# Performance work log

Measured on AMD Instinct MI355X. Metric: run time of the kernel, lower is better.

The kernel has to match this reference:

```python
import jax, jax.numpy as jnp
import numpy as np

HQ, HKV, HD = 32, 8, 64
ROPE_BASE = 10000.0


def _rope_cos_sin(L):
    # torchtune-style interleaved RoPE cache
    theta = 1.0 / (ROPE_BASE ** (jnp.arange(0, HD, 2, dtype=jnp.float32) / HD))  # [HD/2]
    ang = jnp.arange(L, dtype=jnp.float32)[:, None] * theta[None, :]             # [L, HD/2]
    return jnp.cos(ang)[None, :, None, :], jnp.sin(ang)[None, :, None, :]        # [1,L,1,HD/2]


def _apply_rope(t, cos, sin):
    # t: [B, L, H, HD]; pairs are interleaved along last dim
    x = t.reshape(t.shape[:-1] + (HD // 2, 2))
    x0, x1 = x[..., 0], x[..., 1]
    out = jnp.stack([x0 * cos - x1 * sin, x1 * cos + x0 * sin], axis=-1)
    return out.reshape(t.shape)


def setup_inputs() -> dict:
    key = jax.random.key(0)
    k1, k2, k3 = jax.random.split(key, 3)
    B, L, D = 2, 2048, 2048
    x = jax.random.normal(k1, (B, L, D), dtype=jnp.float32)
    w_qkv = jax.random.normal(k2, ((HQ + 2 * HKV) * HD, D), dtype=jnp.float32) * 0.02
    w_o = jax.random.normal(k3, (D, D), dtype=jnp.float32) * 0.02
    return {"x": x, "w_qkv": w_qkv, "w_o": w_o}


def reference(x, w_qkv, w_o):
    B, L, D = x.shape
    G = HQ // HKV  # q heads per kv head
    qkv = x @ w_qkv.T  # [B, L, (HQ+2*HKV)*HD]
    q = qkv[..., : HQ * HD].reshape(B, L, HQ, HD)
    k = qkv[..., HQ * HD : (HQ + HKV) * HD].reshape(B, L, HKV, HD)
    v = qkv[..., (HQ + HKV) * HD :].reshape(B, L, HKV, HD)

    cos, sin = _rope_cos_sin(L)
    q = _apply_rope(q, cos, sin)
    k = _apply_rope(k, cos, sin)

    # GQA: q head h attends with kv head h // G
    q = q.transpose(0, 2, 1, 3).reshape(B, HKV, G, L, HD)
    k = k.transpose(0, 2, 1, 3)  # [B, HKV, L, HD]
    v = v.transpose(0, 2, 1, 3)

    scale = 1.0 / jnp.sqrt(jnp.float32(HD))
    scores = jnp.einsum('bhgqd,bhkd->bhgqk', q, k) * scale  # [B,HKV,G,L,L]
    causal = jnp.tril(jnp.ones((L, L), dtype=bool))
    scores = jnp.where(causal, scores, jnp.finfo(scores.dtype).min)
    attn = jax.nn.softmax(scores, axis=-1)
    y = jnp.einsum('bhgqk,bhkd->bhgqd', attn, v)            # [B,HKV,G,L,HD]
    y = y.reshape(B, HQ, L, HD).transpose(0, 2, 1, 3).reshape(B, L, D)
    return y @ w_o.T
```

## Files before the change

kernel.cpp:

```cpp
#include <hip/hip_runtime.h>

typedef __attribute__((ext_vector_type(8))) short bf16x8;
typedef __attribute__((ext_vector_type(4))) float f32x4;

__device__ __forceinline__ float bf2f(unsigned short u) {
  unsigned int x = ((unsigned int)u) << 16;
  float f; __builtin_memcpy(&f, &x, 4); return f;
}
__device__ __forceinline__ unsigned short f2bf(float f) {
  unsigned int x; __builtin_memcpy(&x, &f, 4);
  unsigned int lsb = (x >> 16) & 1u;
  x += 0x7fffu + lsb;
  return (unsigned short)(x >> 16);
}
__device__ __forceinline__ unsigned short f2bf_trunc(float f) {
  unsigned int x; __builtin_memcpy(&x, &f, 4);
  return (unsigned short)(x >> 16);
}
__device__ __forceinline__ float exp2_raw(float x) {
  float r;
  asm("v_exp_f32 %0, %1" : "=v"(r) : "v"(x));
  return r;
}
__device__ __forceinline__ void gload16(const unsigned short* g, unsigned short* l) {
  __builtin_amdgcn_global_load_lds(
      (const __attribute__((address_space(1))) unsigned int*)g,
      (__attribute__((address_space(3))) unsigned int*)l, 16, 0, 0);
}

__global__ __launch_bounds__(256) void cvt3(const float* __restrict__ x,
                                            const float* __restrict__ wq,
                                            const float* __restrict__ wo,
                                            unsigned short* __restrict__ xb,
                                            unsigned short* __restrict__ wqb,
                                            unsigned short* __restrict__ wob) {
  const int N0 = 1048576, N1 = 786432, N2 = 524288;
  for (int i = blockIdx.x * 256 + threadIdx.x; i < N0 + N1 + N2;
       i += (int)(gridDim.x * 256)) {
    const float* in; unsigned short* out; int j;
    if (i < N0)            { in = x;  out = xb;  j = i; }
    else if (i < N0 + N1)  { in = wq; out = wqb; j = i - N0; }
    else                   { in = wo; out = wob; j = i - N0 - N1; }
    const float4* p = (const float4*)(in + (size_t)j * 8);
    float4 a = p[0], b = p[1];
    union { bf16x8 v; unsigned short u[8]; } o;
    o.u[0] = f2bf(a.x); o.u[1] = f2bf(a.y); o.u[2] = f2bf(a.z); o.u[3] = f2bf(a.w);
    o.u[4] = f2bf(b.x); o.u[5] = f2bf(b.y); o.u[6] = f2bf(b.z); o.u[7] = f2bf(b.w);
    *(bf16x8*)(out + (size_t)j * 8) = o.v;
  }
}

template <int F32OUT>
__global__ __launch_bounds__(256) void gemm_bt(const unsigned short* __restrict__ A,
                                               const unsigned short* __restrict__ B,
                                               void* __restrict__ Cp, int N) {
  __shared__ unsigned short sA[128 * 64];
  __shared__ unsigned short sB[128 * 64];
  const int t = threadIdx.x;
  const int lane = t & 63, w = t >> 6;
  const int wm = w >> 1, wn = w & 1;
  const int l16 = lane & 15, hi = lane >> 4;
  const int m0 = blockIdx.y * 128, n0 = blockIdx.x * 128;

  f32x4 zero = {0.f, 0.f, 0.f, 0.f};
  f32x4 acc[4][4];
#pragma unroll
  for (int mi = 0; mi < 4; ++mi)
#pragma unroll
    for (int ni = 0; ni < 4; ++ni) acc[mi][ni] = zero;

  const unsigned short* gA = A + (size_t)m0 * 2048;
  const unsigned short* gB = B + (size_t)n0 * 2048;

  for (int k0 = 0; k0 < 2048; k0 += 64) {
    __syncthreads();
#pragma unroll
    for (int i = 0; i < 4; ++i) {
      int c = i * 256 + t;
      int row = c >> 3, cb = c & 7;
      gload16(gA + (size_t)row * 2048 + k0 + ((cb ^ (row & 7)) * 8), &sA[c * 8]);
    }
#pragma unroll
    for (int i = 0; i < 4; ++i) {
      int c = i * 256 + t;
      int row = c >> 3, cb = c & 7;
      gload16(gB + (size_t)row * 2048 + k0 + ((cb ^ (row & 7)) * 8), &sB[c * 8]);
    }
    __syncthreads();
#pragma unroll
    for (int kk = 0; kk < 2; ++kk) {
      bf16x8 af[4], bfr[4];
#pragma unroll
      for (int i = 0; i < 4; ++i) {
        int rowa = wm * 64 + i * 16 + l16;
        af[i]  = *(const bf16x8*)&sA[rowa * 64 + (((kk * 4 + hi) ^ (l16 & 7)) * 8)];
        int rowb = wn * 64 + i * 16 + l16;
        bfr[i] = *(const bf16x8*)&sB[rowb * 64 + (((kk * 4 + hi) ^ (l16 & 7)) * 8)];
      }
#pragma unroll
      for (int mi = 0; mi < 4; ++mi)
#pragma unroll
        for (int ni = 0; ni < 4; ++ni)
          acc[mi][ni] = __builtin_amdgcn_mfma_f32_16x16x32_bf16(af[mi], bfr[ni], acc[mi][ni], 0, 0, 0);
    }
  }

  const int rowb = m0 + wm * 64 + hi * 4;
  const int colb = n0 + wn * 64 + l16;
#pragma unroll
  for (int mi = 0; mi < 4; ++mi)
#pragma unroll
    for (int ni = 0; ni < 4; ++ni)
#pragma unroll
      for (int r = 0; r < 4; ++r) {
        size_t idx = (size_t)(rowb + mi * 16 + r) * N + colb + ni * 16;
        if (F32OUT) ((float*)Cp)[idx] = acc[mi][ni][r];
        else        ((unsigned short*)Cp)[idx] = f2bf(acc[mi][ni][r]);
      }
}

__global__ __launch_bounds__(256) void prep(const unsigned short* __restrict__ qkv,
                                            unsigned short* __restrict__ q,
                                            unsigned short* __restrict__ k,
                                            unsigned short* __restrict__ vt) {
  __shared__ unsigned short sT[64 * 72];
  const int bid = blockIdx.x;
  if (bid < 640) {
    int tid = bid * 256 + threadIdx.x;
    int l = tid & 2047;
    int rest = tid >> 11;
    int b = rest & 1;
    int h = rest >> 1;
    const unsigned short* src = qkv + (size_t)(b * 2048 + l) * 3072 + h * 64;
    union { uint4 v[8]; unsigned short u[64]; } buf;
#pragma unroll
    for (int i = 0; i < 8; ++i) buf.v[i] = ((const uint4*)src)[i];
    const float sc = (h < 32) ? 0.125f * 1.44269504088896f : 1.0f;
#pragma unroll
    for (int j = 0; j < 32; ++j) {
      float fr = exp2f(-(float)j * 0.41524101186092033f);
      float ang = (float)l * fr;
      float sn, cs;
      sincosf(ang, &sn, &cs);
      float x0 = bf2f(buf.u[2 * j]), x1 = bf2f(buf.u[2 * j + 1]);
      float y0 = (x0 * cs - x1 * sn) * sc;
      float y1 = (x1 * cs + x0 * sn) * sc;
      buf.u[2 * j] = f2bf(y0);
      buf.u[2 * j + 1] = f2bf(y1);
    }
    unsigned short* dst = (h < 32) ? (q + ((size_t)(b * 32 + h) * 2048 + l) * 64)
                                   : (k + ((size_t)(b * 8 + h - 32) * 2048 + l) * 64);
#pragma unroll
    for (int i = 0; i < 8; ++i) ((uint4*)dst)[i] = buf.v[i];
  } else {
    const int bid2 = bid - 640;
    const int xb = bid2 & 31, bh = bid2 >> 5;
    const int t = threadIdx.x;
    const int b = bh >> 3, h = bh & 7;
    const int l0 = xb * 64;
    const int c = t & 7, i0 = t >> 3;
#pragma unroll
    for (int pp = 0; pp < 2; ++pp) {
      int i = i0 + pp * 32;
      const unsigned short* src =
          qkv + (size_t)(b * 2048 + l0 + i) * 3072 + 2560 + h * 64 + c * 8;
      union { bf16x8 v; unsigned short u[8]; } x;
      x.v = *(const bf16x8*)src;
#pragma unroll
      for (int e = 0; e < 8; ++e) sT[(c * 8 + e) * 72 + i] = x.u[e];
    }
    __syncthreads();
    const int d = t >> 2, ic = (t & 3) * 16;
    unsigned short* dst = vt + ((size_t)(b * 8 + h) * 64 + d) * 2048 + l0 + ic;
    *(bf16x8*)dst = *(const bf16x8*)&sT[d * 72 + ic];
    *(bf16x8*)(dst + 8) = *(const bf16x8*)&sT[d * 72 + ic + 8];
  }
}

__global__ __launch_bounds__(256) void attn(const unsigned short* __restrict__ Q,
                                            const unsigned short* __restrict__ K,
                                            const unsigned short* __restrict__ VT,
                                            unsigned short* __restrict__ Y) {
  __shared__ unsigned short sK[128 * 64];
  __shared__ unsigned short sV[64 * 128];
  __shared__ unsigned short sP[4][32 * 136];
  const int t = threadIdx.x, lane = t & 63, w = t >> 6;
  const int l16 = lane & 15, hi = lane >> 4;
  const int pi = blockIdx.y;
  const int bx = blockIdx.x;
  const int head = ((bx & 7) << 3) | (bx >> 3);
  const int b = head >> 5, hq = head & 31, hkv = hq >> 2;
  const unsigned short* kp = K + (size_t)(b * 8 + hkv) * 2048 * 64;
  const unsigned short* vp = VT + (size_t)(b * 8 + hkv) * 64 * 2048;
  unsigned short* sPw = sP[w];
  f32x4 zero = {0.f, 0.f, 0.f, 0.f};
  union { bf16x8 v; unsigned short u[8]; } ones_u;
#pragma unroll
  for (int j = 0; j < 8; ++j) ones_u.u[j] = 0x3F80;
  const bf16x8 ones = ones_u.v;

#pragma unroll
  for (int phase = 0; phase < 2; ++phase) {
    const int qb = phase ? (15 - pi) : pi;
    const int q0 = qb * 128 + w * 32;
    const unsigned short* qp = Q + ((size_t)(b * 32 + hq) * 2048 + q0) * 64;

    bf16x8 qf[2][2];
#pragma unroll
    for (int mi = 0; mi < 2; ++mi)
#pragma unroll
      for (int ks = 0; ks < 2; ++ks)
        qf[mi][ks] = *(const bf16x8*)(qp + (size_t)(mi * 16 + l16) * 64 + ks * 32 + hi * 8);

    f32x4 o[2][4];
    f32x4 os[2];
#pragma unroll
    for (int mi = 0; mi < 2; ++mi) {
#pragma unroll
      for (int ni = 0; ni < 4; ++ni) o[mi][ni] = zero;
      os[mi] = zero;
    }

    const int nt = qb + 1;
    for (int tt = 0; tt < nt; ++tt) {
      const int c0 = tt * 128;
      __syncthreads();
#pragma unroll
      for (int i = 0; i < 4; ++i) {
        int c = i * 256 + t;
        int row = c >> 3, cb = c & 7;
        gload16(kp + (size_t)(c0 + row) * 64 + ((cb ^ (row & 7)) * 8), &sK[c * 8]);
      }
#pragma unroll
      for (int i = 0; i < 4; ++i) {
        int c = i * 256 + t;
        int d = c >> 4, cb = c & 15;
        gload16(vp + (size_t)d * 2048 + c0 + ((cb ^ (d & 15)) * 8), &sV[c * 8]);
      }
      __syncthreads();

#pragma unroll
      for (int h = 0; h < 2; ++h) {
        const int c0h = c0 + h * 64;
        if (c0h > q0) break;
        f32x4 sc[2][4];
#pragma unroll
        for (int mi = 0; mi < 2; ++mi)
#pragma unroll
          for (int ni = 0; ni < 4; ++ni) sc[mi][ni] = zero;
#pragma unroll
        for (int ni = 0; ni < 4; ++ni) {
          const int krow = h * 64 + ni * 16 + l16;
          bf16x8 k0f = *(const bf16x8*)&sK[krow * 64 + ((hi ^ (l16 & 7)) * 8)];
          bf16x8 k1f = *(const bf16x8*)&sK[krow * 64 + (((4 + hi) ^ (l16 & 7)) * 8)];
#pragma unroll
          for (int mi = 0; mi < 2; ++mi) {
            sc[mi][ni] = __builtin_amdgcn_mfma_f32_16x16x32_bf16(qf[mi][0], k0f, sc[mi][ni], 0, 0, 0);
            sc[mi][ni] = __builtin_amdgcn_mfma_f32_16x16x32_bf16(qf[mi][1], k1f, sc[mi][ni], 0, 0, 0);
          }
        }
        if (c0h + 64 > q0) {
#pragma unroll
          for (int mi = 0; mi < 2; ++mi)
#pragma unroll
            for (int ni = 0; ni < 4; ++ni)
#pragma unroll
              for (int r = 0; r < 4; ++r) {
                int col = c0h + ni * 16 + l16;
                int row = q0 + mi * 16 + hi * 4 + r;
                if (col > row) sc[mi][ni][r] = -1e30f;
              }
        }
#pragma unroll
        for (int mi = 0; mi < 2; ++mi)
#pragma unroll
          for (int ni = 0; ni < 4; ++ni)
#pragma unroll
            for (int r = 0; r < 4; ++r) {
              float p = exp2_raw(sc[mi][ni][r]);
              sPw[(mi * 16 + hi * 4 + r) * 136 + h * 64 + ni * 16 + l16] = f2bf_trunc(p);
            }
      }
#pragma unroll
      for (int ks = 0; ks < 4; ++ks) {
        if (c0 + ks * 32 > q0) break;
        bf16x8 pa[2];
#pragma unroll
        for (int mi = 0; mi < 2; ++mi) {
          pa[mi] = *(const bf16x8*)&sPw[(mi * 16 + l16) * 136 + ks * 32 + hi * 8];
          os[mi] = __builtin_amdgcn_mfma_f32_16x16x32_bf16(pa[mi], ones, os[mi], 0, 0, 0);
        }
#pragma unroll
        for (int ni = 0; ni < 4; ++ni) {
          const int d = ni * 16 + l16;
          bf16x8 vb = *(const bf16x8*)&sV[d * 128 + (((ks * 4 + hi) ^ l16) * 8)];
#pragma unroll
          for (int mi = 0; mi < 2; ++mi)
            o[mi][ni] = __builtin_amdgcn_mfma_f32_16x16x32_bf16(pa[mi], vb, o[mi][ni], 0, 0, 0);
        }
      }
    }
#pragma unroll
    for (int mi = 0; mi < 2; ++mi) {
      float inv[4];
#pragma unroll
      for (int r = 0; r < 4; ++r) inv[r] = 1.f / os[mi][r];
#pragma unroll
      for (int ni = 0; ni < 4; ++ni)
#pragma unroll
        for (int r = 0; r < 4; ++r) {
          int row = q0 + mi * 16 + hi * 4 + r;
          Y[(size_t)(b * 2048 + row) * 2048 + hq * 64 + ni * 16 + l16] =
              f2bf(o[mi][ni][r] * inv[r]);
        }
    }
  }
}

extern "C" void kernel_launch(void* const* d_in, const int* in_sizes, int n_in,
                              void* d_out, int out_size, void* d_ws, size_t ws_size,
                              hipStream_t stream) {
  const float* x    = (const float*)d_in[0];
  const float* wqkv = (const float*)d_in[1];
  const float* wo   = (const float*)d_in[2];
  float* out = (float*)d_out;

  char* ws = (char*)d_ws;
  unsigned short* xb   = (unsigned short*)(ws);
  unsigned short* wqb  = (unsigned short*)(ws + 16777216);
  unsigned short* wob  = (unsigned short*)(ws + 29360128);
  unsigned short* qkvb = (unsigned short*)(ws + 37748736);
  unsigned short* qb   = (unsigned short*)(ws + 62914560);
  unsigned short* kb   = (unsigned short*)(ws + 79691776);
  unsigned short* vtb  = (unsigned short*)(ws + 83886080);
  unsigned short* yb = xb;

  cvt3<<<2048, 256, 0, stream>>>(x, wqkv, wo, xb, wqb, wob);
  gemm_bt<0><<<dim3(3072 / 128, 4096 / 128), 256, 0, stream>>>(xb, wqb, qkvb, 3072);
  prep<<<1152, 256, 0, stream>>>(qkvb, qb, kb, vtb);
  attn<<<dim3(64, 8), 256, 0, stream>>>(qb, kb, vtb, yb);
  gemm_bt<1><<<dim3(2048 / 128, 4096 / 128), 256, 0, stream>>>(yb, wob, out, 2048);
}
```

Baseline: 199.5 us.

## Keep attention probabilities in registers by computing transposed scores

Swaps the QK^T MFMA operand order so each lane holds four consecutive key positions for one query row. That matches the A-operand layout of the 16x16x16 bf16 MFMA, so P can feed the PV product directly from registers. This removes the per-wave shared-memory P buffer, its writes and reads, and uses packed bf16 conversion via v_cvt_pk_bf16_f32. In exchange it uses the half-depth K=16 MFMA, which issues twice as many PV and row-sum MFMA instructions, reads V in narrower 4-element loads, and changes the causal-mask indexing.

```diff
diff --git a/kernel.cpp b/kernel.cpp
--- a/kernel.cpp
+++ b/kernel.cpp
@@ -1,6 +1,7 @@
 #include <hip/hip_runtime.h>
 
 typedef __attribute__((ext_vector_type(8))) short bf16x8;
+typedef __attribute__((ext_vector_type(4))) short bf16x4;
 typedef __attribute__((ext_vector_type(4))) float f32x4;
 
 __device__ __forceinline__ float bf2f(unsigned short u) {
@@ -13,15 +14,28 @@
   x += 0x7fffu + lsb;
   return (unsigned short)(x >> 16);
 }
-__device__ __forceinline__ unsigned short f2bf_trunc(float f) {
-  unsigned int x; __builtin_memcpy(&x, &f, 4);
-  return (unsigned short)(x >> 16);
-}
 __device__ __forceinline__ float exp2_raw(float x) {
   float r;
   asm("v_exp_f32 %0, %1" : "=v"(r) : "v"(x));
   return r;
 }
+__device__ __forceinline__ unsigned int cvtpk_bf16(float lo, float hi) {
+  unsigned int r;
+  asm("v_cvt_pk_bf16_f32 %0, %1, %2" : "=v"(r) : "v"(lo), "v"(hi));
+  return r;
+}
+#if __has_builtin(__builtin_amdgcn_mfma_f32_16x16x16bf16_1k)
+__device__ __forceinline__ f32x4 mfma16(bf16x4 a, bf16x4 b, f32x4 c) {
+  return __builtin_amdgcn_mfma_f32_16x16x16bf16_1k(a, b, c, 0, 0, 0);
+}
+#else
+__device__ __forceinline__ f32x4 mfma16(bf16x4 a, bf16x4 b, f32x4 c) {
+  f32x4 d;
+  asm volatile("v_mfma_f32_16x16x16_bf16 %0, %1, %2, %3"
+               : "=v"(d) : "v"(a), "v"(b), "v"(c));
+  return d;
+}
+#endif
 __device__ __forceinline__ void gload16(const unsigned short* g, unsigned short* l) {
   __builtin_amdgcn_global_load_lds(
       (const __attribute__((address_space(1))) unsigned int*)g,
@@ -183,7 +197,6 @@
                                             unsigned short* __restrict__ Y) {
   __shared__ unsigned short sK[128 * 64];
   __shared__ unsigned short sV[64 * 128];
-  __shared__ unsigned short sP[4][32 * 136];
   const int t = threadIdx.x, lane = t & 63, w = t >> 6;
   const int l16 = lane & 15, hi = lane >> 4;
   const int pi = blockIdx.y;
@@ -192,12 +205,11 @@
   const int b = head >> 5, hq = head & 31, hkv = hq >> 2;
   const unsigned short* kp = K + (size_t)(b * 8 + hkv) * 2048 * 64;
   const unsigned short* vp = VT + (size_t)(b * 8 + hkv) * 64 * 2048;
-  unsigned short* sPw = sP[w];
   f32x4 zero = {0.f, 0.f, 0.f, 0.f};
-  union { bf16x8 v; unsigned short u[8]; } ones_u;
-#pragma unroll
-  for (int j = 0; j < 8; ++j) ones_u.u[j] = 0x3F80;
-  const bf16x8 ones = ones_u.v;
+  union { bf16x4 v; unsigned short u[4]; } ones_u;
+#pragma unroll
+  for (int j = 0; j < 4; ++j) ones_u.u[j] = 0x3F80;
+  const bf16x4 ones4 = ones_u.v;
 
 #pragma unroll
   for (int phase = 0; phase < 2; ++phase) {
@@ -255,8 +267,8 @@
           bf16x8 k1f = *(const bf16x8*)&sK[krow * 64 + (((4 + hi) ^ (l16 & 7)) * 8)];
 #pragma unroll
           for (int mi = 0; mi < 2; ++mi) {
-            sc[mi][ni] = __builtin_amdgcn_mfma_f32_16x16x32_bf16(qf[mi][0], k0f, sc[mi][ni], 0, 0, 0);
-            sc[mi][ni] = __builtin_amdgcn_mfma_f32_16x16x32_bf16(qf[mi][1], k1f, sc[mi][ni], 0, 0, 0);
+            sc[mi][ni] = __builtin_amdgcn_mfma_f32_16x16x32_bf16(k0f, qf[mi][0], sc[mi][ni], 0, 0, 0);
+            sc[mi][ni] = __builtin_amdgcn_mfma_f32_16x16x32_bf16(k1f, qf[mi][1], sc[mi][ni], 0, 0, 0);
           }
         }
         if (c0h + 64 > q0) {
@@ -266,37 +278,36 @@
             for (int ni = 0; ni < 4; ++ni)
 #pragma unroll
               for (int r = 0; r < 4; ++r) {
-                int col = c0h + ni * 16 + l16;
-                int row = q0 + mi * 16 + hi * 4 + r;
-                if (col > row) sc[mi][ni][r] = -1e30f;
+                int kv = c0h + ni * 16 + hi * 4 + r;
+                int qq = q0 + mi * 16 + l16;
+                if (kv > qq) sc[mi][ni][r] = -1e30f;
               }
         }
 #pragma unroll
-        for (int mi = 0; mi < 2; ++mi)
-#pragma unroll
-          for (int ni = 0; ni < 4; ++ni)
-#pragma unroll
-            for (int r = 0; r < 4; ++r) {
-              float p = exp2_raw(sc[mi][ni][r]);
-              sPw[(mi * 16 + hi * 4 + r) * 136 + h * 64 + ni * 16 + l16] = f2bf_trunc(p);
-            }
-      }
-#pragma unroll
-      for (int ks = 0; ks < 4; ++ks) {
-        if (c0 + ks * 32 > q0) break;
-        bf16x8 pa[2];
-#pragma unroll
-        for (int mi = 0; mi < 2; ++mi) {
-          pa[mi] = *(const bf16x8*)&sPw[(mi * 16 + l16) * 136 + ks * 32 + hi * 8];
-          os[mi] = __builtin_amdgcn_mfma_f32_16x16x32_bf16(pa[mi], ones, os[mi], 0, 0, 0);
-        }
-#pragma unroll
         for (int ni = 0; ni < 4; ++ni) {
-          const int d = ni * 16 + l16;
-          bf16x8 vb = *(const bf16x8*)&sV[d * 128 + (((ks * 4 + hi) ^ l16) * 8)];
-#pragma unroll
-          for (int mi = 0; mi < 2; ++mi)
-            o[mi][ni] = __builtin_amdgcn_mfma_f32_16x16x32_bf16(pa[mi], vb, o[mi][ni], 0, 0, 0);
+          if (c0h + ni * 16 > q0 + 16) break;
+          bf16x4 pa[2];
+#pragma unroll
+          for (int mi = 0; mi < 2; ++mi) {
+            float p0 = exp2_raw(sc[mi][ni][0]);
+            float p1 = exp2_raw(sc[mi][ni][1]);
+            float p2 = exp2_raw(sc[mi][ni][2]);
+            float p3 = exp2_raw(sc[mi][ni][3]);
+            union { unsigned int w2[2]; bf16x4 v; } pk;
+            pk.w2[0] = cvtpk_bf16(p0, p1);
+            pk.w2[1] = cvtpk_bf16(p2, p3);
+            pa[mi] = pk.v;
+            os[mi] = mfma16(pa[mi], ones4, os[mi]);
+          }
+          const int cb = h * 8 + ni * 2 + (hi >> 1);
+#pragma unroll
+          for (int nd = 0; nd < 4; ++nd) {
+            const int d = nd * 16 + l16;
+            bf16x4 vb = *(const bf16x4*)&sV[d * 128 + ((cb ^ (d & 15)) * 8) + (hi & 1) * 4];
+#pragma unroll
+            for (int mi = 0; mi < 2; ++mi)
+              o[mi][nd] = mfma16(pa[mi], vb, o[mi][nd]);
+          }
         }
       }
     }
```

Result: slower. 206.0 us (+3.2%).
